# Kernel optimization log

Measured on AMD Instinct MI355X. Metric: run time of the kernel, lower is better.

Reference implementation:

```python
import jax, jax.numpy as jnp
import numpy as np

FH, FW, CIN, COUT = 5, 5, 3, 16
PATCH = FH * FW * CIN  # 75
ALPHA = 1.0


def smooth_max(xk, axis):
    # alpha-softmax smooth maximum: sum(x * exp(alpha*x)) / sum(exp(alpha*x))
    w = jax.nn.softmax(ALPHA * xk, axis=axis)
    return jnp.sum(w * xk, axis=axis)


def setup_inputs() -> dict:
    key = jax.random.key(0)
    k_x, k_k1, k_k2 = jax.random.split(key, 3)
    B, Hout, Wout = 2, 220, 220
    x = jax.random.normal(k_x, (B, PATCH, Hout, Wout), dtype=jnp.float32)
    # xavier_uniform for kernel shape (fh, fw, cin, cout): fan_in=fh*fw*cin? torch treats
    # dims [..0]=fan stuff; a small uniform init is faithful enough for a numeric baseline.
    lim = float(np.sqrt(6.0 / (PATCH + COUT)))
    k1 = jax.random.uniform(k_k1, (FH, FW, CIN, COUT), jnp.float32, -lim, lim)
    k2 = jax.random.uniform(k_k2, (FH, FW, CIN, COUT), jnp.float32, -lim, lim)
    bias = jnp.zeros((COUT,), dtype=jnp.float32)
    return {"x": x, "k1": k1, "k2": k2, "bias": bias}


def reference(x, k1, k2, bias):
    # x: (B, patch_dim, Hout, Wout) unfolded patches
    k1f = k1.reshape(PATCH, COUT)  # (patch_dim, out_ch)
    k2f = k2.reshape(PATCH, COUT)
    # broadcast add: (B, patch_dim, out_ch, H, W)
    xk1 = x[:, :, None, :, :] + k1f[None, :, :, None, None]
    y11 = smooth_max(xk1, axis=1)  # (B, out_ch, H, W)
    xk2 = (-x)[:, :, None, :, :] + k2f[None, :, :, None, None]
    y22 = smooth_max(xk2, axis=1)
    return y11 + y22 + bias[None, :, None, None]
```

## Files before the change

kernel.cpp:

```cpp
#include <hip/hip_runtime.h>

#define HWD    48400
#define PATCHD 75
#define NPOS   96800
#define KPAD   96

typedef __attribute__((ext_vector_type(8))) _Float16 f16x8;
typedef __attribute__((ext_vector_type(2))) __fp16   h16x2;
typedef __attribute__((ext_vector_type(4))) float    f32x4;

union U2 { h16x2 h; unsigned u; };
union UF { unsigned u[4]; f16x8 v; };

__global__ void smorph_build_tables(const float* __restrict__ k1,
                                    const float* __restrict__ k2,
                                    _Float16* __restrict__ tbl)
{
    int i = (int)blockIdx.x * 256 + (int)threadIdx.x;
    if (i >= 2 * 16 * KPAD) return;
    int dir = i / (16 * KPAD);
    int r   = i - dir * (16 * KPAD);
    int c   = r / KPAD;
    int k   = r - c * KPAD;
    const float* kw = dir ? k2 : k1;
    float a = 0.f, b = 0.f;
    if (k < PATCHD) {
        float w = kw[k * 16 + c];
        float e = __expf(w);
        a = e;
        b = w * e;
    }
    tbl[(dir * 2 + 0) * (16 * KPAD) + c * KPAD + k] = (_Float16)a;
    tbl[(dir * 2 + 1) * (16 * KPAD) + c * KPAD + k] = (_Float16)b;
}

__global__ __launch_bounds__(256, 4)
void smorph_mfma3(const float* __restrict__ x,
                  const _Float16* __restrict__ tbl,
                  const float* __restrict__ bias,
                  float* __restrict__ out)
{
    const int tid = (int)threadIdx.x;
    const int l   = tid & 63;
    const int w   = tid >> 6;
    const int g   = l >> 4;
    const int c   = l & 15;
    const int p0  = (int)blockIdx.x * 64 + w * 16;
    if (p0 >= NPOS) return;
    const int b   = (p0 >= HWD) ? 1 : 0;
    const int hw0 = p0 - b * HWD;

    const _Float16* tA1 = tbl + 0 * (16 * KPAD) + c * KPAD;
    const _Float16* tB1 = tbl + 1 * (16 * KPAD) + c * KPAD;
    const _Float16* tA2 = tbl + 2 * (16 * KPAD) + c * KPAD;
    const _Float16* tB2 = tbl + 3 * (16 * KPAD) + c * KPAD;

    const float* xb = x + (size_t)b * PATCHD * HWD + hw0 + c;

    f32x4 aN1 = {0.f,0.f,0.f,0.f}, aD1 = {0.f,0.f,0.f,0.f};
    f32x4 aN2 = {0.f,0.f,0.f,0.f}, aD2 = {0.f,0.f,0.f,0.f};

    #pragma unroll 1
    for (int s = 0; s < 3; ++s) {
        const int kbase = 32 * s + 8 * g;
        const float* xs = xb + (size_t)kbase * HWD;

        float xv[8], E[8], R[8];
        #pragma unroll
        for (int j = 0; j < 8; ++j) {
            const int k = kbase + j;
            xv[j] = (k < PATCHD) ? xs[(size_t)j * HWD] : 0.f;
        }
        #pragma unroll
        for (int j = 0; j < 8; ++j) {
            E[j] = __expf(xv[j]);
            R[j] = __expf(-xv[j]);
        }

        UF fEx, fE, fRx, fR;
        #pragma unroll
        for (int jp = 0; jp < 4; ++jp) {
            U2 q;
            q.h = __builtin_amdgcn_cvt_pkrtz(E[2*jp] * xv[2*jp], E[2*jp+1] * xv[2*jp+1]);
            fEx.u[jp] = q.u;
            q.h = __builtin_amdgcn_cvt_pkrtz(E[2*jp], E[2*jp+1]);
            fE.u[jp]  = q.u;
            q.h = __builtin_amdgcn_cvt_pkrtz(R[2*jp] * -xv[2*jp], R[2*jp+1] * -xv[2*jp+1]);
            fRx.u[jp] = q.u;
            q.h = __builtin_amdgcn_cvt_pkrtz(R[2*jp], R[2*jp+1]);
            fR.u[jp]  = q.u;
        }

        UF a1f, b1f, a2f, b2f;
        #pragma unroll
        for (int jp = 0; jp < 4; ++jp) {
            a1f.u[jp] = *(const unsigned*)(tA1 + kbase + 2 * jp);
            b1f.u[jp] = *(const unsigned*)(tB1 + kbase + 2 * jp);
            a2f.u[jp] = *(const unsigned*)(tA2 + kbase + 2 * jp);
            b2f.u[jp] = *(const unsigned*)(tB2 + kbase + 2 * jp);
        }

        aN1 = __builtin_amdgcn_mfma_f32_16x16x32_f16(a1f.v, fEx.v, aN1, 0, 0, 0);
        aN1 = __builtin_amdgcn_mfma_f32_16x16x32_f16(b1f.v, fE.v,  aN1, 0, 0, 0);
        aD1 = __builtin_amdgcn_mfma_f32_16x16x32_f16(a1f.v, fE.v,  aD1, 0, 0, 0);
        aN2 = __builtin_amdgcn_mfma_f32_16x16x32_f16(a2f.v, fRx.v, aN2, 0, 0, 0);
        aN2 = __builtin_amdgcn_mfma_f32_16x16x32_f16(b2f.v, fR.v,  aN2, 0, 0, 0);
        aD2 = __builtin_amdgcn_mfma_f32_16x16x32_f16(a2f.v, fR.v,  aD2, 0, 0, 0);
    }

    float* ob = out + ((size_t)(b * 16 + 4 * g)) * HWD + hw0 + c;
    #pragma unroll
    for (int r = 0; r < 4; ++r) {
        const float y = aN1[r] * __builtin_amdgcn_rcpf(aD1[r])
                      + aN2[r] * __builtin_amdgcn_rcpf(aD2[r])
                      + bias[4 * g + r];
        ob[(size_t)r * HWD] = y;
    }
}

extern "C" void kernel_launch(void* const* d_in, const int* in_sizes, int n_in,
                              void* d_out, int out_size, void* d_ws, size_t ws_size,
                              hipStream_t stream)
{
    const float* x    = (const float*)d_in[0];
    const float* k1   = (const float*)d_in[1];
    const float* k2   = (const float*)d_in[2];
    const float* bias = (const float*)d_in[3];
    float* out = (float*)d_out;
    _Float16* tbl = (_Float16*)d_ws;

    smorph_build_tables<<<(2 * 16 * KPAD + 255) / 256, 256, 0, stream>>>(k1, k2, tbl);
    smorph_mfma3<<<(NPOS + 63) / 64, 256, 0, stream>>>(x, tbl, bias, out);
}
```

Baseline: 19.13 us.

## Stage x tiles into LDS via async global_load_lds with double buffering

Replaces the per-lane strided global loads of x with 16-byte global_load_lds transfers into a double-buffered shared tile, so each stage's load overlaps the previous stage's exp/MFMA work. The table fragments for all three stages are hoisted into registers up front, and the bias is read as one float4. It also clamps the last block's base so the staging loads stay in bounds. In exchange it adds LDS use, block-wide barriers and more live registers, which could reduce occupancy.

```diff
diff --git a/kernel.cpp b/kernel.cpp
--- a/kernel.cpp
+++ b/kernel.cpp
@@ -11,6 +11,10 @@
 
 union U2 { h16x2 h; unsigned u; };
 union UF { unsigned u[4]; f16x8 v; };
+
+#define GLOAD_LDS16(g, l) __builtin_amdgcn_global_load_lds(               \
+    (const __attribute__((address_space(1))) void*)(g),                   \
+    (__attribute__((address_space(3))) void*)(l), 16, 0, 0)
 
 __global__ void smorph_build_tables(const float* __restrict__ k1,
                                     const float* __restrict__ k2,
@@ -35,86 +39,112 @@
 }
 
 __global__ __launch_bounds__(256, 4)
-void smorph_mfma3(const float* __restrict__ x,
+void smorph_mfma4(const float* __restrict__ x,
                   const _Float16* __restrict__ tbl,
                   const float* __restrict__ bias,
                   float* __restrict__ out)
 {
+    __shared__ __align__(16) float sX[2][32][64];
+
     const int tid = (int)threadIdx.x;
     const int l   = tid & 63;
     const int w   = tid >> 6;
     const int g   = l >> 4;
     const int c   = l & 15;
-    const int p0  = (int)blockIdx.x * 64 + w * 16;
-    if (p0 >= NPOS) return;
-    const int b   = (p0 >= HWD) ? 1 : 0;
-    const int hw0 = p0 - b * HWD;
 
-    const _Float16* tA1 = tbl + 0 * (16 * KPAD) + c * KPAD;
-    const _Float16* tB1 = tbl + 1 * (16 * KPAD) + c * KPAD;
-    const _Float16* tA2 = tbl + 2 * (16 * KPAD) + c * KPAD;
-    const _Float16* tB2 = tbl + 3 * (16 * KPAD) + c * KPAD;
+    int p0_blk = (int)blockIdx.x * 64;
+    if (p0_blk > NPOS - 64) p0_blk = NPOS - 64;
 
-    const float* xb = x + (size_t)b * PATCHD * HWD + hw0 + c;
+    const int ps   = p0_blk + 4 * c;
+    const int sb   = (ps >= HWD) ? 1 : 0;
+    const float* sg = x + (size_t)sb * PATCHD * HWD + (ps - sb * HWD);
+
+    #define STAGE(buf, s)                                                     \
+        {                                                                     \
+            _Pragma("unroll")                                                 \
+            for (int i = 0; i < 2; ++i) {                                     \
+                const int row = (2 * w + i) * 4 + g;                          \
+                const int k   = 32 * (s) + row;                               \
+                if (k < PATCHD)                                               \
+                    GLOAD_LDS16(sg + (size_t)k * HWD, &sX[buf][(2 * w + i) * 4][0]); \
+            }                                                                 \
+        }
+
+    const int pcol = w * 16 + c;
+    const int p0w  = p0_blk + w * 16;
+    const int b    = (p0w >= HWD) ? 1 : 0;
+    const int hw0  = p0w - b * HWD;
+
+    UF Ta1[3], Tb1[3], Ta2[3], Tb2[3];
+    const _Float16* t0 = tbl + c * KPAD;
+    #pragma unroll
+    for (int s = 0; s < 3; ++s)
+        #pragma unroll
+        for (int jp = 0; jp < 4; ++jp) {
+            const int off = 32 * s + 8 * g + 2 * jp;
+            Ta1[s].u[jp] = *(const unsigned*)(t0 + 0 * 16 * KPAD + off);
+            Tb1[s].u[jp] = *(const unsigned*)(t0 + 1 * 16 * KPAD + off);
+            Ta2[s].u[jp] = *(const unsigned*)(t0 + 2 * 16 * KPAD + off);
+            Tb2[s].u[jp] = *(const unsigned*)(t0 + 3 * 16 * KPAD + off);
+        }
 
     f32x4 aN1 = {0.f,0.f,0.f,0.f}, aD1 = {0.f,0.f,0.f,0.f};
     f32x4 aN2 = {0.f,0.f,0.f,0.f}, aD2 = {0.f,0.f,0.f,0.f};
 
-    #pragma unroll 1
-    for (int s = 0; s < 3; ++s) {
-        const int kbase = 32 * s + 8 * g;
-        const float* xs = xb + (size_t)kbase * HWD;
-
-        float xv[8], E[8], R[8];
-        #pragma unroll
-        for (int j = 0; j < 8; ++j) {
-            const int k = kbase + j;
-            xv[j] = (k < PATCHD) ? xs[(size_t)j * HWD] : 0.f;
-        }
-        #pragma unroll
-        for (int j = 0; j < 8; ++j) {
-            E[j] = __expf(xv[j]);
-            R[j] = __expf(-xv[j]);
+    #define COMPUTE(buf, s)                                                   \
+        {                                                                     \
+            const float* lp = &sX[buf][8 * g][pcol];                          \
+            float xv[8];                                                      \
+            _Pragma("unroll")                                                 \
+            for (int j = 0; j < 8; ++j) xv[j] = lp[j * 64];                   \
+            _Pragma("unroll")                                                 \
+            for (int j = 0; j < 8; ++j)                                       \
+                if (32 * (s) + 8 * g + j >= PATCHD) xv[j] = 0.f;              \
+            float E[8], R[8];                                                 \
+            _Pragma("unroll")                                                 \
+            for (int j = 0; j < 8; ++j) { E[j] = __expf(xv[j]); R[j] = __expf(-xv[j]); } \
+            UF fEx, fE, fRx, fR;                                              \
+            _Pragma("unroll")                                                 \
+            for (int jp = 0; jp < 4; ++jp) {                                  \
+                U2 q;                                                         \
+                q.h = __builtin_amdgcn_cvt_pkrtz(E[2*jp] * xv[2*jp], E[2*jp+1] * xv[2*jp+1]);   \
+                fEx.u[jp] = q.u;                                              \
+                q.h = __builtin_amdgcn_cvt_pkrtz(E[2*jp], E[2*jp+1]);         \
+                fE.u[jp]  = q.u;                                              \
+                q.h = __builtin_amdgcn_cvt_pkrtz(-R[2*jp] * xv[2*jp], -R[2*jp+1] * xv[2*jp+1]); \
+                fRx.u[jp] = q.u;                                              \
+                q.h = __builtin_amdgcn_cvt_pkrtz(R[2*jp], R[2*jp+1]);         \
+                fR.u[jp]  = q.u;                                              \
+            }                                                                 \
+            aN1 = __builtin_amdgcn_mfma_f32_16x16x32_f16(Ta1[s].v, fEx.v, aN1, 0, 0, 0); \
+            aN1 = __builtin_amdgcn_mfma_f32_16x16x32_f16(Tb1[s].v, fE.v,  aN1, 0, 0, 0); \
+            aD1 = __builtin_amdgcn_mfma_f32_16x16x32_f16(Ta1[s].v, fE.v,  aD1, 0, 0, 0); \
+            aN2 = __builtin_amdgcn_mfma_f32_16x16x32_f16(Ta2[s].v, fRx.v, aN2, 0, 0, 0); \
+            aN2 = __builtin_amdgcn_mfma_f32_16x16x32_f16(Tb2[s].v, fR.v,  aN2, 0, 0, 0); \
+            aD2 = __builtin_amdgcn_mfma_f32_16x16x32_f16(Ta2[s].v, fR.v,  aD2, 0, 0, 0); \
         }
 
-        UF fEx, fE, fRx, fR;
-        #pragma unroll
-        for (int jp = 0; jp < 4; ++jp) {
-            U2 q;
-            q.h = __builtin_amdgcn_cvt_pkrtz(E[2*jp] * xv[2*jp], E[2*jp+1] * xv[2*jp+1]);
-            fEx.u[jp] = q.u;
-            q.h = __builtin_amdgcn_cvt_pkrtz(E[2*jp], E[2*jp+1]);
-            fE.u[jp]  = q.u;
-            q.h = __builtin_amdgcn_cvt_pkrtz(R[2*jp] * -xv[2*jp], R[2*jp+1] * -xv[2*jp+1]);
-            fRx.u[jp] = q.u;
-            q.h = __builtin_amdgcn_cvt_pkrtz(R[2*jp], R[2*jp+1]);
-            fR.u[jp]  = q.u;
-        }
+    STAGE(0, 0);
+    __syncthreads();
+    STAGE(1, 1);
+    COMPUTE(0, 0);
+    __syncthreads();
+    STAGE(0, 2);
+    COMPUTE(1, 1);
+    __syncthreads();
+    COMPUTE(0, 2);
 
-        UF a1f, b1f, a2f, b2f;
-        #pragma unroll
-        for (int jp = 0; jp < 4; ++jp) {
-            a1f.u[jp] = *(const unsigned*)(tA1 + kbase + 2 * jp);
-            b1f.u[jp] = *(const unsigned*)(tB1 + kbase + 2 * jp);
-            a2f.u[jp] = *(const unsigned*)(tA2 + kbase + 2 * jp);
-            b2f.u[jp] = *(const unsigned*)(tB2 + kbase + 2 * jp);
-        }
-
-        aN1 = __builtin_amdgcn_mfma_f32_16x16x32_f16(a1f.v, fEx.v, aN1, 0, 0, 0);
-        aN1 = __builtin_amdgcn_mfma_f32_16x16x32_f16(b1f.v, fE.v,  aN1, 0, 0, 0);
-        aD1 = __builtin_amdgcn_mfma_f32_16x16x32_f16(a1f.v, fE.v,  aD1, 0, 0, 0);
-        aN2 = __builtin_amdgcn_mfma_f32_16x16x32_f16(a2f.v, fRx.v, aN2, 0, 0, 0);
-        aN2 = __builtin_amdgcn_mfma_f32_16x16x32_f16(b2f.v, fR.v,  aN2, 0, 0, 0);
-        aD2 = __builtin_amdgcn_mfma_f32_16x16x32_f16(a2f.v, fR.v,  aD2, 0, 0, 0);
-    }
-
+    const float4 bsv = *(const float4*)(bias + 4 * g);
     float* ob = out + ((size_t)(b * 16 + 4 * g)) * HWD + hw0 + c;
-    #pragma unroll
-    for (int r = 0; r < 4; ++r) {
-        const float y = aN1[r] * __builtin_amdgcn_rcpf(aD1[r])
-                      + aN2[r] * __builtin_amdgcn_rcpf(aD2[r])
-                      + bias[4 * g + r];
-        ob[(size_t)r * HWD] = y;
+    {
+        const float y0 = aN1[0] * __builtin_amdgcn_rcpf(aD1[0]) + aN2[0] * __builtin_amdgcn_rcpf(aD2[0]) + bsv.x;
+        const float y1 = aN1[1] * __builtin_amdgcn_rcpf(aD1[1]) + aN2[1] * __builtin_amdgcn_rcpf(aD2[1]) + bsv.y;
+        const float y2 = aN1[2] * __builtin_amdgcn_rcpf(aD1[2]) + aN2[2] * __builtin_amdgcn_rcpf(aD2[2]) + bsv.z;
+        const float y3 = aN1[3] * __builtin_amdgcn_rcpf(aD1[3]) + aN2[3] * __builtin_amdgcn_rcpf(aD2[3]) + bsv.w;
+        ob[0 * (size_t)HWD] = y0;
+        ob[1 * (size_t)HWD] = y1;
+        ob[2 * (size_t)HWD] = y2;
+        ob[3 * (size_t)HWD] = y3;
     }
 }
 
@@ -130,5 +160,5 @@
     _Float16* tbl = (_Float16*)d_ws;
 
     smorph_build_tables<<<(2 * 16 * KPAD + 255) / 256, 256, 0, stream>>>(k1, k2, tbl);
-    smorph_mfma3<<<(NPOS + 63) / 64, 256, 0, stream>>>(x, tbl, bias, out);
+    smorph_mfma4<<<(NPOS + 63) / 64, 256, 0, stream>>>(x, tbl, bias, out);
 }
```

Result: no change. 19.36 us (+1.2%).
